# Performance work log

Measured on AMD Instinct MI355X. Metric: run time of the kernel, lower is better.

## Reference

```python
import jax, jax.numpy as jnp
import numpy as np


def setup_inputs() -> dict:
    key = jax.random.key(0)
    k1, k2, k3, k4 = jax.random.split(key, 4)
    N, D, B = 300000, 256, 512
    x = jax.random.normal(k1, (N, D), dtype=jnp.float32)
    batch = jnp.sort(jax.random.randint(k2, (N,), 0, B, dtype=jnp.int64))
    W1 = jax.random.normal(k3, (D, D // 2), dtype=jnp.float32) / np.sqrt(D)
    b1 = jnp.zeros((D // 2,), dtype=jnp.float32)
    W2 = jax.random.normal(k4, (D // 2, 1), dtype=jnp.float32) / np.sqrt(D // 2)
    b2 = jnp.zeros((1,), dtype=jnp.float32)
    return {"x": x, "batch": batch, "num_segments": B,
            "W1": W1, "b1": b1, "W2": W2, "b2": b2}


def reference(x, batch, num_segments, W1, b1, W2, b2):
    # attention MLP: Linear -> ReLU -> Linear, output [N, 1]
    h = jax.nn.relu(x @ W1 + b1)
    scores = h @ W2 + b2                       # [N, 1]
    # softmax over ALL nodes (dim=0), as in the original module
    w = jax.nn.softmax(scores, axis=0)          # [N, 1]
    # weighted segment-sum per graph; empty segments yield zero rows
    pooled = jax.ops.segment_sum(x * w, batch, num_segments=num_segments)
    return pooled                                # [num_segments, D]
```

## Files before the change

kernel.cpp:

```cpp
#include <hip/hip_runtime.h>
#include <math.h>

typedef __attribute__((ext_vector_type(8))) short bf16x8;
typedef __attribute__((ext_vector_type(4))) float f32x4;

constexpr int D = 256;
constexpr int H = 128;
constexpr int KSTEPS = D / 32;
constexpr int BM = 128;
constexpr int NPB3 = 64;

__device__ __forceinline__ unsigned int enc_f(float f) {
  unsigned int b = __float_as_uint(f);
  return (b & 0x80000000u) ? ~b : (b | 0x80000000u);
}
__device__ __forceinline__ float dec_f(unsigned int u) {
  return __uint_as_float((u & 0x80000000u) ? (u ^ 0x80000000u) : ~u);
}
__device__ __forceinline__ float trunc_bf(float a) {
  return __uint_as_float(__float_as_uint(a) & 0xFFFF0000u);
}
__device__ __forceinline__ unsigned int pack2_bf(float a, float b) {
  return (__float_as_uint(a) >> 16) | (__float_as_uint(b) & 0xFFFF0000u);
}

union FragU { uint4 u; bf16x8 f; };

__device__ __forceinline__ void gload16(const void* g, void* l) {
  __builtin_amdgcn_global_load_lds(
      (const __attribute__((address_space(1))) unsigned int*)g,
      (__attribute__((address_space(3))) unsigned int*)l, 16, 0, 0);
}
__device__ __forceinline__ void block_sync() {
  asm volatile("" ::: "memory");
  __builtin_amdgcn_s_barrier();
  asm volatile("" ::: "memory");
}

extern "C" __global__ void __launch_bounds__(256)
k_init(float* __restrict__ out, int out_size, unsigned int* __restrict__ gmax,
       float* __restrict__ zacc)
{
  const int i = blockIdx.x * 256 + threadIdx.x;
  if (i < out_size) out[i] = 0.0f;
  if (i == 0) { *gmax = 0u; *zacc = 0.0f; }
}

extern "C" __global__ void __launch_bounds__(256)
k_pack(const float* __restrict__ W1, uint4* __restrict__ phi,
       uint4* __restrict__ plo)
{
  const int g = blockIdx.x * 256 + threadIdx.x;
  const int c = g >> 9, ht = (g >> 6) & 7, l = g & 63;
  const int kbase = c * 32 + (l >> 4) * 8;
  const int col = ht * 16 + (l & 15);
  float v[8], lo[8];
#pragma unroll
  for (int i = 0; i < 8; ++i) {
    v[i] = W1[(size_t)(kbase + i) * H + col];
    lo[i] = v[i] - trunc_bf(v[i]);
  }
  uint4 h4, l4;
  h4.x = pack2_bf(v[0], v[1]); h4.y = pack2_bf(v[2], v[3]);
  h4.z = pack2_bf(v[4], v[5]); h4.w = pack2_bf(v[6], v[7]);
  l4.x = pack2_bf(lo[0], lo[1]); l4.y = pack2_bf(lo[2], lo[3]);
  l4.z = pack2_bf(lo[4], lo[5]); l4.w = pack2_bf(lo[6], lo[7]);
  phi[g] = h4; plo[g] = l4;
}

extern "C" __global__ void __launch_bounds__(256, 2)
k_scores_mfma(const float* __restrict__ x, const uint4* __restrict__ phi,
              const uint4* __restrict__ plo, const float* __restrict__ b1,
              const float* __restrict__ W2, const float* __restrict__ b2,
              float* __restrict__ scores, unsigned int* __restrict__ gmax, int N)
{
  __shared__ float4 xplane[2][1024];
  __shared__ uint4 btile[2][1024];
  __shared__ float sred[2][BM];

  const int t = threadIdx.x;
  const int l = t & 63;
  const int w = t >> 6;
  const int lg = l >> 4;
  const int lr = l & 15;
  const int rg = w >> 1;
  const int cg = w & 1;
  const int n0 = blockIdx.x * BM;

  const char* xb = (const char*)x;
  const char* phib = (const char*)phi;
  const char* plob = (const char*)plo;

  auto STAGE = [&](int buf, int c) {
#pragma unroll
    for (int i = 0; i < 4; ++i) {
      const int plane = i * 4 + w;
      const int g = plane >> 1, p = plane & 1;
      const int srow = min(n0 + g * 16 + lr, N - 1);
      gload16(xb + (size_t)srow * 1024 + c * 128 + lg * 32 + p * 16,
              (char*)&xplane[buf][plane * 64 + l]);
    }
    char* bd = (char*)&btile[buf][0];
#pragma unroll
    for (int i = 0; i < 2; ++i) {
      const int off = i * 4096 + t * 16;
      gload16(phib + c * 8192 + off, bd + off);
      gload16(plob + c * 8192 + off, bd + 8192 + off);
    }
  };

  f32x4 acc[4][4] = {};

  STAGE(0, 0);
#pragma unroll 1
  for (int c = 0; c < KSTEPS; ++c) {
    const int cur = c & 1;
    if (c + 1 < KSTEPS) {
      STAGE(cur ^ 1, c + 1);
      asm volatile("s_waitcnt vmcnt(8)" ::: "memory");
    } else {
      asm volatile("s_waitcnt vmcnt(0)" ::: "memory");
    }
    block_sync();

    FragU bhi[4], blo[4];
#pragma unroll
    for (int h = 0; h < 4; ++h) {
      const int ht = cg * 4 + h;
      bhi[h].u = btile[cur][ht * 64 + l];
      blo[h].u = btile[cur][512 + ht * 64 + l];
    }
#pragma unroll
    for (int s = 0; s < 4; ++s) {
      const int g = rg * 4 + s;
      const float4 u0 = xplane[cur][(g * 2 + 0) * 64 + l];
      const float4 u1 = xplane[cur][(g * 2 + 1) * 64 + l];
      float v[8], lo[8];
      v[0] = u0.x; v[1] = u0.y; v[2] = u0.z; v[3] = u0.w;
      v[4] = u1.x; v[5] = u1.y; v[6] = u1.z; v[7] = u1.w;
#pragma unroll
      for (int i = 0; i < 8; ++i) lo[i] = v[i] - trunc_bf(v[i]);
      FragU ahi, alo;
      ahi.u.x = pack2_bf(v[0], v[1]);  ahi.u.y = pack2_bf(v[2], v[3]);
      ahi.u.z = pack2_bf(v[4], v[5]);  ahi.u.w = pack2_bf(v[6], v[7]);
      alo.u.x = pack2_bf(lo[0], lo[1]); alo.u.y = pack2_bf(lo[2], lo[3]);
      alo.u.z = pack2_bf(lo[4], lo[5]); alo.u.w = pack2_bf(lo[6], lo[7]);
#pragma unroll
      for (int h = 0; h < 4; ++h) {
        acc[s][h] = __builtin_amdgcn_mfma_f32_16x16x32_bf16(ahi.f, bhi[h].f, acc[s][h], 0, 0, 0);
        acc[s][h] = __builtin_amdgcn_mfma_f32_16x16x32_bf16(ahi.f, blo[h].f, acc[s][h], 0, 0, 0);
        acc[s][h] = __builtin_amdgcn_mfma_f32_16x16x32_bf16(alo.f, bhi[h].f, acc[s][h], 0, 0, 0);
      }
    }
    block_sync();
  }

  float bvv[4], wvv[4];
#pragma unroll
  for (int h = 0; h < 4; ++h) {
    const int col = (cg * 4 + h) * 16 + lr;
    bvv[h] = b1[col];
    wvv[h] = W2[col];
  }
#pragma unroll
  for (int s = 0; s < 4; ++s) {
#pragma unroll
    for (int r = 0; r < 4; ++r) {
      float p = 0.0f;
#pragma unroll
      for (int h = 0; h < 4; ++h)
        p = fmaf(fmaxf(acc[s][h][r] + bvv[h], 0.0f), wvv[h], p);
#pragma unroll
      for (int off = 1; off < 16; off <<= 1) p += __shfl_xor(p, off, 64);
      if (lr == 0) sred[cg][rg * 64 + s * 16 + lg * 4 + r] = p;
    }
  }
  __syncthreads();
  if (cg == 0) {
    const int row = rg * 64 + l;
    const int node = n0 + row;
    const float sc = sred[0][row] + sred[1][row] + b2[0];
    float mym = -INFINITY;
    if (node < N) { scores[node] = sc; mym = sc; }
#pragma unroll
    for (int off = 1; off < 64; off <<= 1)
      mym = fmaxf(mym, __shfl_xor(mym, off, 64));
    if (l == 0) atomicMax(gmax, enc_f(mym));
  }
}

extern "C" __global__ void __launch_bounds__(256)
k_expsum(const float* __restrict__ scores, const unsigned int* __restrict__ gmax,
         float* __restrict__ zacc, int N)
{
  const float m = dec_f(*gmax);
  float sum = 0.0f;
  for (int i = blockIdx.x * blockDim.x + threadIdx.x; i < N;
       i += gridDim.x * blockDim.x)
    sum += __expf(scores[i] - m);
#pragma unroll
  for (int off = 32; off > 0; off >>= 1) sum += __shfl_down(sum, off, 64);
  __shared__ float wred[4];
  if ((threadIdx.x & 63) == 0) wred[threadIdx.x >> 6] = sum;
  __syncthreads();
  if (threadIdx.x == 0)
    atomicAdd(zacc, wred[0] + wred[1] + wred[2] + wred[3]);
}

extern "C" __global__ void __launch_bounds__(64)
k_pool(const float* __restrict__ x, const int* __restrict__ batch,
       const float* __restrict__ scores, const unsigned int* __restrict__ gmax,
       const float* __restrict__ zacc, float* __restrict__ out, int N)
{
  const int t = threadIdx.x;
  const int n0 = blockIdx.x * NPB3;
  const int n1 = min(n0 + NPB3, N);
  if (n0 >= n1) return;
  const float m = dec_f(*gmax);
  const float invZ = 1.0f / (*zacc);

  float4 acc = make_float4(0.f, 0.f, 0.f, 0.f);
  int bprev = batch[n0];
  for (int n = n0; n < n1; ++n) {
    const int b = batch[n];
    if (b != bprev) {
      float* o = out + (size_t)bprev * D + t * 4;
      atomicAdd(o + 0, acc.x); atomicAdd(o + 1, acc.y);
      atomicAdd(o + 2, acc.z); atomicAdd(o + 3, acc.w);
      acc = make_float4(0.f, 0.f, 0.f, 0.f);
      bprev = b;
    }
    const float wgt = __expf(scores[n] - m) * invZ;
    const float4 xv = *reinterpret_cast<const float4*>(x + (size_t)n * D + t * 4);
    acc.x = fmaf(xv.x, wgt, acc.x);
    acc.y = fmaf(xv.y, wgt, acc.y);
    acc.z = fmaf(xv.z, wgt, acc.z);
    acc.w = fmaf(xv.w, wgt, acc.w);
  }
  float* o = out + (size_t)bprev * D + t * 4;
  atomicAdd(o + 0, acc.x); atomicAdd(o + 1, acc.y);
  atomicAdd(o + 2, acc.z); atomicAdd(o + 3, acc.w);
}

extern "C" void kernel_launch(void* const* d_in, const int* in_sizes, int n_in,
                              void* d_out, int out_size, void* d_ws, size_t ws_size,
                              hipStream_t stream)
{
  const float* x     = (const float*)d_in[0];
  const int*   batch = (const int*)d_in[1];
  const float* W1 = (const float*)d_in[3];
  const float* b1 = (const float*)d_in[4];
  const float* W2 = (const float*)d_in[5];
  const float* b2 = (const float*)d_in[6];
  const int N = in_sizes[1];

  unsigned int* gmax = (unsigned int*)d_ws;
  float* zacc        = (float*)((char*)d_ws + 64);
  uint4* phi         = (uint4*)((char*)d_ws + 256);
  uint4* plo         = (uint4*)((char*)d_ws + 256 + 65536);
  float* scores      = (float*)((char*)d_ws + 256 + 131072);

  k_init<<<(out_size + 255) / 256, 256, 0, stream>>>((float*)d_out, out_size,
                                                     gmax, zacc);
  k_pack<<<16, 256, 0, stream>>>(W1, phi, plo);

  const int g1 = (N + BM - 1) / BM;
  k_scores_mfma<<<g1, 256, 0, stream>>>(x, phi, plo, b1, W2, b2, scores, gmax, N);

  int g2 = (N + 255) / 256; if (g2 > 2048) g2 = 2048;
  k_expsum<<<g2, 256, 0, stream>>>(scores, gmax, zacc, N);

  const int g3 = (N + NPB3 - 1) / NPB3;
  k_pool<<<g3, 64, 0, stream>>>(x, batch, scores, gmax, zacc, (float*)d_out, N);
}
```

Before: 200.6 us.

## Fuse score MLP, softmax and segment pooling into one kernel

Merges the MFMA score kernel, the exp-sum kernel and the pooling kernel into one kernel. Each block computes exp(score) for its 128 rows and keeps the weights in LDS. It adds them into a global Z and pools those same x rows right away, while they are likely still in cache. A small final kernel divides the output by Z. The global max subtraction is dropped, which removes a pass over all scores but risks exp overflow for large scores. W1 fragments are now read straight from global into registers rather than staged in LDS, and occupancy is raised to 3 blocks per SM.

```diff
diff --git a/kernel.cpp b/kernel.cpp
--- a/kernel.cpp
+++ b/kernel.cpp
@@ -8,15 +8,7 @@
 constexpr int H = 128;
 constexpr int KSTEPS = D / 32;
 constexpr int BM = 128;
-constexpr int NPB3 = 64;
-
-__device__ __forceinline__ unsigned int enc_f(float f) {
-  unsigned int b = __float_as_uint(f);
-  return (b & 0x80000000u) ? ~b : (b | 0x80000000u);
-}
-__device__ __forceinline__ float dec_f(unsigned int u) {
-  return __uint_as_float((u & 0x80000000u) ? (u ^ 0x80000000u) : ~u);
-}
+
 __device__ __forceinline__ float trunc_bf(float a) {
   return __uint_as_float(__float_as_uint(a) & 0xFFFF0000u);
 }
@@ -38,12 +30,11 @@
 }
 
 extern "C" __global__ void __launch_bounds__(256)
-k_init(float* __restrict__ out, int out_size, unsigned int* __restrict__ gmax,
-       float* __restrict__ zacc)
+k_init(float* __restrict__ out, int out_size, float* __restrict__ zacc)
 {
   const int i = blockIdx.x * 256 + threadIdx.x;
   if (i < out_size) out[i] = 0.0f;
-  if (i == 0) { *gmax = 0u; *zacc = 0.0f; }
+  if (i == 0) *zacc = 0.0f;
 }
 
 extern "C" __global__ void __launch_bounds__(256)
@@ -68,15 +59,16 @@
   phi[g] = h4; plo[g] = l4;
 }
 
-extern "C" __global__ void __launch_bounds__(256, 2)
-k_scores_mfma(const float* __restrict__ x, const uint4* __restrict__ phi,
-              const uint4* __restrict__ plo, const float* __restrict__ b1,
-              const float* __restrict__ W2, const float* __restrict__ b2,
-              float* __restrict__ scores, unsigned int* __restrict__ gmax, int N)
+extern "C" __global__ void __launch_bounds__(256, 3)
+k_fused(const float* __restrict__ x, const int* __restrict__ batch,
+        const uint4* __restrict__ phi, const uint4* __restrict__ plo,
+        const float* __restrict__ b1, const float* __restrict__ W2,
+        const float* __restrict__ b2, float* __restrict__ out,
+        float* __restrict__ zacc, int N)
 {
   __shared__ float4 xplane[2][1024];
-  __shared__ uint4 btile[2][1024];
   __shared__ float sred[2][BM];
+  __shared__ float wlds[BM];
 
   const int t = threadIdx.x;
   const int l = t & 63;
@@ -88,8 +80,6 @@
   const int n0 = blockIdx.x * BM;
 
   const char* xb = (const char*)x;
-  const char* phib = (const char*)phi;
-  const char* plob = (const char*)plo;
 
   auto STAGE = [&](int buf, int c) {
 #pragma unroll
@@ -100,13 +90,6 @@
       gload16(xb + (size_t)srow * 1024 + c * 128 + lg * 32 + p * 16,
               (char*)&xplane[buf][plane * 64 + l]);
     }
-    char* bd = (char*)&btile[buf][0];
-#pragma unroll
-    for (int i = 0; i < 2; ++i) {
-      const int off = i * 4096 + t * 16;
-      gload16(phib + c * 8192 + off, bd + off);
-      gload16(plob + c * 8192 + off, bd + 8192 + off);
-    }
   };
 
   f32x4 acc[4][4] = {};
@@ -115,21 +98,21 @@
 #pragma unroll 1
   for (int c = 0; c < KSTEPS; ++c) {
     const int cur = c & 1;
+    FragU bhi[4], blo[4];
+#pragma unroll
+    for (int h = 0; h < 4; ++h) {
+      const int ht = cg * 4 + h;
+      bhi[h].u = phi[(c * 8 + ht) * 64 + l];
+      blo[h].u = plo[(c * 8 + ht) * 64 + l];
+    }
     if (c + 1 < KSTEPS) {
       STAGE(cur ^ 1, c + 1);
-      asm volatile("s_waitcnt vmcnt(8)" ::: "memory");
+      asm volatile("s_waitcnt vmcnt(4)" ::: "memory");
     } else {
       asm volatile("s_waitcnt vmcnt(0)" ::: "memory");
     }
     block_sync();
 
-    FragU bhi[4], blo[4];
-#pragma unroll
-    for (int h = 0; h < 4; ++h) {
-      const int ht = cg * 4 + h;
-      bhi[h].u = btile[cur][ht * 64 + l];
-      blo[h].u = btile[cur][512 + ht * 64 + l];
-    }
 #pragma unroll
     for (int s = 0; s < 4; ++s) {
       const int g = rg * 4 + s;
@@ -180,66 +163,49 @@
     const int row = rg * 64 + l;
     const int node = n0 + row;
     const float sc = sred[0][row] + sred[1][row] + b2[0];
-    float mym = -INFINITY;
-    if (node < N) { scores[node] = sc; mym = sc; }
-#pragma unroll
-    for (int off = 1; off < 64; off <<= 1)
-      mym = fmaxf(mym, __shfl_xor(mym, off, 64));
-    if (l == 0) atomicMax(gmax, enc_f(mym));
+    const float wgt = (node < N) ? __expf(sc) : 0.0f;
+    wlds[row] = wgt;
+    float zs = wgt;
+#pragma unroll
+    for (int off = 1; off < 64; off <<= 1) zs += __shfl_xor(zs, off, 64);
+    if (l == 0) atomicAdd(zacc, zs);
+  }
+  __syncthreads();
+
+  {
+    const int nStart = n0 + w * 32;
+    const int nEnd = min(nStart + 32, N);
+    if (nStart < nEnd) {
+      float4 a4 = make_float4(0.f, 0.f, 0.f, 0.f);
+      int bprev = batch[nStart];
+      for (int n = nStart; n < nEnd; ++n) {
+        const int b = batch[n];
+        if (b != bprev) {
+          float* o = out + (size_t)bprev * D + l * 4;
+          atomicAdd(o + 0, a4.x); atomicAdd(o + 1, a4.y);
+          atomicAdd(o + 2, a4.z); atomicAdd(o + 3, a4.w);
+          a4 = make_float4(0.f, 0.f, 0.f, 0.f);
+          bprev = b;
+        }
+        const float wgt = wlds[n - n0];
+        const float4 xv = *reinterpret_cast<const float4*>(x + (size_t)n * D + l * 4);
+        a4.x = fmaf(xv.x, wgt, a4.x);
+        a4.y = fmaf(xv.y, wgt, a4.y);
+        a4.z = fmaf(xv.z, wgt, a4.z);
+        a4.w = fmaf(xv.w, wgt, a4.w);
+      }
+      float* o = out + (size_t)bprev * D + l * 4;
+      atomicAdd(o + 0, a4.x); atomicAdd(o + 1, a4.y);
+      atomicAdd(o + 2, a4.z); atomicAdd(o + 3, a4.w);
+    }
   }
 }
 
 extern "C" __global__ void __launch_bounds__(256)
-k_expsum(const float* __restrict__ scores, const unsigned int* __restrict__ gmax,
-         float* __restrict__ zacc, int N)
-{
-  const float m = dec_f(*gmax);
-  float sum = 0.0f;
-  for (int i = blockIdx.x * blockDim.x + threadIdx.x; i < N;
-       i += gridDim.x * blockDim.x)
-    sum += __expf(scores[i] - m);
-#pragma unroll
-  for (int off = 32; off > 0; off >>= 1) sum += __shfl_down(sum, off, 64);
-  __shared__ float wred[4];
-  if ((threadIdx.x & 63) == 0) wred[threadIdx.x >> 6] = sum;
-  __syncthreads();
-  if (threadIdx.x == 0)
-    atomicAdd(zacc, wred[0] + wred[1] + wred[2] + wred[3]);
-}
-
-extern "C" __global__ void __launch_bounds__(64)
-k_pool(const float* __restrict__ x, const int* __restrict__ batch,
-       const float* __restrict__ scores, const unsigned int* __restrict__ gmax,
-       const float* __restrict__ zacc, float* __restrict__ out, int N)
-{
-  const int t = threadIdx.x;
-  const int n0 = blockIdx.x * NPB3;
-  const int n1 = min(n0 + NPB3, N);
-  if (n0 >= n1) return;
-  const float m = dec_f(*gmax);
-  const float invZ = 1.0f / (*zacc);
-
-  float4 acc = make_float4(0.f, 0.f, 0.f, 0.f);
-  int bprev = batch[n0];
-  for (int n = n0; n < n1; ++n) {
-    const int b = batch[n];
-    if (b != bprev) {
-      float* o = out + (size_t)bprev * D + t * 4;
-      atomicAdd(o + 0, acc.x); atomicAdd(o + 1, acc.y);
-      atomicAdd(o + 2, acc.z); atomicAdd(o + 3, acc.w);
-      acc = make_float4(0.f, 0.f, 0.f, 0.f);
-      bprev = b;
-    }
-    const float wgt = __expf(scores[n] - m) * invZ;
-    const float4 xv = *reinterpret_cast<const float4*>(x + (size_t)n * D + t * 4);
-    acc.x = fmaf(xv.x, wgt, acc.x);
-    acc.y = fmaf(xv.y, wgt, acc.y);
-    acc.z = fmaf(xv.z, wgt, acc.z);
-    acc.w = fmaf(xv.w, wgt, acc.w);
-  }
-  float* o = out + (size_t)bprev * D + t * 4;
-  atomicAdd(o + 0, acc.x); atomicAdd(o + 1, acc.y);
-  atomicAdd(o + 2, acc.z); atomicAdd(o + 3, acc.w);
+k_finish(float* __restrict__ out, const float* __restrict__ zacc, int size)
+{
+  const int i = blockIdx.x * 256 + threadIdx.x;
+  if (i < size) out[i] *= (1.0f / *zacc);
 }
 
 extern "C" void kernel_launch(void* const* d_in, const int* in_sizes, int n_in,
@@ -254,22 +220,16 @@
   const float* b2 = (const float*)d_in[6];
   const int N = in_sizes[1];
 
-  unsigned int* gmax = (unsigned int*)d_ws;
-  float* zacc        = (float*)((char*)d_ws + 64);
-  uint4* phi         = (uint4*)((char*)d_ws + 256);
-  uint4* plo         = (uint4*)((char*)d_ws + 256 + 65536);
-  float* scores      = (float*)((char*)d_ws + 256 + 131072);
-
-  k_init<<<(out_size + 255) / 256, 256, 0, stream>>>((float*)d_out, out_size,
-                                                     gmax, zacc);
+  float* zacc = (float*)d_ws;
+  uint4* phi  = (uint4*)((char*)d_ws + 256);
+  uint4* plo  = (uint4*)((char*)d_ws + 256 + 65536);
+
+  k_init<<<(out_size + 255) / 256, 256, 0, stream>>>((float*)d_out, out_size, zacc);
   k_pack<<<16, 256, 0, stream>>>(W1, phi, plo);
 
   const int g1 = (N + BM - 1) / BM;
-  k_scores_mfma<<<g1, 256, 0, stream>>>(x, phi, plo, b1, W2, b2, scores, gmax, N);
-
-  int g2 = (N + 255) / 256; if (g2 > 2048) g2 = 2048;
-  k_expsum<<<g2, 256, 0, stream>>>(scores, gmax, zacc, N);
-
-  const int g3 = (N + NPB3 - 1) / NPB3;
-  k_pool<<<g3, 64, 0, stream>>>(x, batch, scores, gmax, zacc, (float*)d_out, N);
-}
+  k_fused<<<g1, 256, 0, stream>>>(x, batch, phi, plo, b1, W2, b2,
+                                  (float*)d_out, zacc, N);
+
+  k_finish<<<(out_size + 255) / 256, 256, 0, stream>>>((float*)d_out, zacc, out_size);
+}
```

Result: faster. 181.6 us (-9.5%).
